# Optimization experiments

Measured on AMD Instinct MI355X. Metric: run time of the kernel, lower is better.

Reference implementation:

```python
import jax, jax.numpy as jnp
import numpy as np
import math

B_GRAPHS = 256
L_NODES = 64
N_NODES = B_GRAPHS * L_NODES
N_EDGES = N_NODES * 4
HEADS = 8
D_INNER = 512
N_DAGS = 1
DIAMETER = 64


def setup_inputs() -> dict:
    key = jax.random.key(0)
    ks = jax.random.split(key, 8)
    x = jax.random.normal(ks[0], (N_NODES, D_INNER), jnp.float32)
    B = jax.random.normal(ks[1], (N_NODES, D_INNER), jnp.float32)
    C = jax.random.normal(ks[2], (N_NODES, D_INNER), jnp.float32)
    dt = jax.random.normal(ks[3], (N_NODES, N_DAGS * HEADS * 2), jnp.float32)
    dt_edge = jax.random.normal(ks[4], (N_EDGES, N_DAGS * HEADS), jnp.float32)
    # DAG edges: within each graph, src_local < dst_local (gap 1..7) -> strictly upper triangular
    u = jax.random.randint(ks[5], (N_EDGES,), 0, L_NODES - 1)
    gap = jax.random.randint(ks[6], (N_EDGES,), 1, 8)
    v = jnp.minimum(u + gap, L_NODES - 1)
    graph = jnp.arange(N_EDGES) // (N_EDGES // B_GRAPHS)
    edge_index = jnp.stack([graph * L_NODES + u, graph * L_NODES + v]).astype(jnp.int32)
    data_batch = (jnp.arange(N_NODES) // L_NODES).astype(jnp.int32)
    dag_masks = jnp.ones((N_DAGS, N_EDGES), jnp.float32)
    # dt_bias init as in module __init__ (inverse softplus of dt in [1e-3, 1e-1])
    rng = np.random.default_rng(0)
    dtv = np.exp(rng.uniform(size=(HEADS,)) * (math.log(0.1) - math.log(0.001)) + math.log(0.001))
    dtv = np.clip(dtv, 1e-4, None)
    dt_bias = jnp.asarray(dtv + np.log(-np.expm1(-dtv)), jnp.float32)
    D = jnp.ones((HEADS,), jnp.float32)
    return dict(x=x, B=B, C=C, dt=dt, dt_edge=dt_edge, dt_bias=dt_bias, D=D,
                dag_masks=dag_masks, edge_index=edge_index, data_batch=data_batch,
                diameter=DIAMETER)


def _repeated_squaring_inverse(A, diam):
    # (I - A)^{-1} = prod_k (I + A^{2^k}) for nilpotent A; O(log diam) matmuls
    j = 2 ** int(math.ceil(math.log2(diam)))
    I = jnp.eye(A.shape[-1], dtype=A.dtype)
    last = A
    M = I + A
    for _ in range(2, int(math.log2(j)) + 1):
        last = last @ last
        M = M @ (I + last)
    return M


def reference(x, B, C, dt, dt_edge, dt_bias, D, dag_masks, edge_index, data_batch, diameter):
    N, din = x.shape
    g, E = dag_masks.shape
    n = dt_bias.shape[0]
    b = int(data_batch[-1]) + 1
    l = N // b  # equal-size graphs -> dense batching is a reshape, mask all-True
    h = din // n
    src, dst = edge_index[0], edge_index[1]

    # dt_node: (N, g*n*c) -> (c, g, n, N); softplus(dt + bias)
    c = dt.shape[1] // (g * n)
    dtn = dt.reshape(N, g, n, c).transpose(3, 1, 2, 0)
    dtn = jax.nn.softplus(dtn + dt_bias[None, None, :, None])
    dte = dt_edge.reshape(E, g, n).transpose(1, 2, 0)  # (g,n,E)
    dte = jax.nn.softplus(dte + dt_bias[None, :, None])

    dt_s, dt_t = dtn[0], dtn[1]
    dt_sum = (dt_s[:, :, src] + dt_t[:, :, dst] + dte) / np.sqrt(3.0)  # (g,n,E)
    dt_exp = jnp.exp(-dt_sum)
    msk = dag_masks[:, None, :]
    dt_sum = dt_sum * msk
    dt_exp = dt_exp * msk

    # dense adjacency with per-edge attrs; note 'b l1 l2 (g n) -> b g n l2 l1' transpose
    b_e = src // l
    sl = src % l
    dl = dst % l
    attr = dt_exp.transpose(2, 0, 1).reshape(E, g * n)
    adj = jnp.zeros((b, l, l, g * n), x.dtype).at[b_e, sl, dl].add(attr)
    A = adj.reshape(b, l, l, g, n).transpose(0, 3, 4, 2, 1)  # (b,g,n,l,l)

    # normalize_mat: sqrt outer product of in-degree counts, clamped at 1
    ec = jnp.zeros((g, N), x.dtype).at[:, dst].add(dag_masks)
    ec_dense = ec.T.reshape(b, l, g)
    outer = jnp.sqrt(jnp.einsum('blg,btg->bglt', ec_dense, ec_dense))
    outer = jnp.where(outer < 1.0, 1.0, outer)
    A = A / outer[:, :, None]

    dnorm = jnp.zeros((g, n, N), x.dtype).at[:, :, dst].add(dt_sum)
    dnorm = dnorm.transpose(2, 0, 1).reshape(b, l, g, n).transpose(0, 2, 3, 1)  # (b,g,n,l)

    A2 = A.reshape(b, g * n, l, l).astype(jnp.float32)
    L = _repeated_squaring_inverse(A2, int(diameter))
    L = L.reshape(b, g, n, l, l) * dnorm[..., None]

    x4 = x.reshape(b, l, n, h).transpose(0, 2, 1, 3)  # (b,n,l,h)
    B3 = B.reshape(b, l, -1)
    C3 = C.reshape(b, l, -1)
    # y = einsum(C,L,B,x) with B/C broadcast over (g,n): fold C.B^T into L
    CB = jnp.einsum('bld,btd->blt', C3, B3)
    M = L * CB[:, None, None]
    y = jnp.einsum('bgnlt,bnth->bgnlh', M, x4)
    y = y + x4[:, None] * D[None, None, :, None, None]
    y = y.transpose(0, 3, 1, 2, 4).reshape(N, g, n * h)  # b g n l h -> (N, g, n*h)
    y = y.sum(axis=1) / np.sqrt(g)
    return y
```

## Files before the change

kernel.cpp:

```cpp
#include <hip/hip_runtime.h>
#include <math.h>

#define NGRAPH 256
#define LNODE  64
#define HEADS  8
#define DIN    512
#define EPG    256
#define NEDGE  65536

__device__ __forceinline__ float softplusf(float v) {
    return (v > 20.f) ? v : log1pf(expf(v));
}

__global__ __launch_bounds__(256) void cb_kernel(const float* __restrict__ Bm,
                                                 const float* __restrict__ Cm,
                                                 float* __restrict__ CBt,
                                                 int dper) {
    int b = blockIdx.x;
    int slice = blockIdx.y;
    __shared__ float Rs[64 * 68];
    __shared__ float Ls[64 * 68];
    int tid = threadIdx.x;
    int ti = tid >> 4, tj = tid & 15;
    float acc[4][4] = {};
    const float* Bg = Bm + (size_t)b * 64 * DIN;
    const float* Cg = Cm + (size_t)b * 64 * DIN;
    int d_lo = slice * dper;
    for (int d0 = d_lo; d0 < d_lo + dper; d0 += 64) {
        __syncthreads();
        #pragma unroll
        for (int k = 0; k < 4; ++k) {
            int f = k * 256 + tid;
            int row = f >> 4;
            int c4 = (f & 15) << 2;
            float4 bv = *(const float4*)(Bg + row * DIN + d0 + c4);
            float4 cv = *(const float4*)(Cg + row * DIN + d0 + c4);
            *(float4*)(Rs + row * 68 + c4) = bv;
            *(float4*)(Ls + row * 68 + c4) = cv;
        }
        __syncthreads();
        for (int d = 0; d < 64; d += 4) {
            float4 rr[4], cc[4];
            #pragma unroll
            for (int r = 0; r < 4; ++r) rr[r] = *(const float4*)(Rs + (4 * ti + r) * 68 + d);
            #pragma unroll
            for (int c = 0; c < 4; ++c) cc[c] = *(const float4*)(Ls + (4 * tj + c) * 68 + d);
            #pragma unroll
            for (int r = 0; r < 4; ++r)
                #pragma unroll
                for (int c = 0; c < 4; ++c)
                    acc[r][c] += rr[r].x * cc[c].x + rr[r].y * cc[c].y +
                                 rr[r].z * cc[c].z + rr[r].w * cc[c].w;
        }
    }
    float* outp = CBt + ((size_t)slice * NGRAPH + b) * 4096;
    #pragma unroll
    for (int r = 0; r < 4; ++r) {
        float4 v = make_float4(acc[r][0], acc[r][1], acc[r][2], acc[r][3]);
        *(float4*)(outp + (4 * ti + r) * 64 + 4 * tj) = v;
    }
}

__global__ __launch_bounds__(256, 4) void main_kernel(const float* __restrict__ x,
                                                      const float* __restrict__ dt,
                                                      const float* __restrict__ dt_edge,
                                                      const float* __restrict__ dt_bias,
                                                      const float* __restrict__ Dp,
                                                      const float* __restrict__ dag_masks,
                                                      const int* __restrict__ edge_index,
                                                      const float* __restrict__ CBt,
                                                      float* __restrict__ out,
                                                      int nslice) {
    int b = blockIdx.x;
    int head = blockIdx.y;
    __shared__ float Ab[64 * 8];
    __shared__ float Mt[64 * 68];
    __shared__ float Xs[64 * 64];
    __shared__ float dnsh[64];
    __shared__ float ecsh[64];
    __shared__ float dts[64];
    __shared__ float dtt[64];
    int tid = threadIdx.x;

    int t4 = tid >> 2;
    int ib = (tid & 3) << 4;
    float4 cbsum[4];
    #pragma unroll
    for (int g = 0; g < 4; ++g) cbsum[g] = make_float4(0.f, 0.f, 0.f, 0.f);
    for (int s = 0; s < nslice; ++s) {
        const float* p = CBt + ((size_t)s * NGRAPH + b) * 4096 + t4 * 64 + ib;
        float4 v0 = *(const float4*)(p + 0);
        float4 v1 = *(const float4*)(p + 4);
        float4 v2 = *(const float4*)(p + 8);
        float4 v3 = *(const float4*)(p + 12);
        cbsum[0].x += v0.x; cbsum[0].y += v0.y; cbsum[0].z += v0.z; cbsum[0].w += v0.w;
        cbsum[1].x += v1.x; cbsum[1].y += v1.y; cbsum[1].z += v1.z; cbsum[1].w += v1.w;
        cbsum[2].x += v2.x; cbsum[2].y += v2.y; cbsum[2].z += v2.z; cbsum[2].w += v2.w;
        cbsum[3].x += v3.x; cbsum[3].y += v3.y; cbsum[3].z += v3.z; cbsum[3].w += v3.w;
    }

    const float* xg0 = x + ((size_t)b * 64) * DIN + head * 64;
    #pragma unroll
    for (int k = 0; k < 4; ++k) {
        int s = k * 256 + tid;
        int row = s >> 4;
        int c4 = (s & 15) << 2;
        float4 v = *(const float4*)(xg0 + (size_t)row * DIN + c4);
        *(float4*)(Xs + row * 64 + c4) = v;
    }

    for (int k = tid; k < 512; k += 256) Ab[k] = 0.f;
    float bias = dt_bias[head];
    if (tid < 64) {
        dnsh[tid] = 0.f;
        ecsh[tid] = 0.f;
        int node = b * 64 + tid;
        dts[tid] = softplusf(dt[node * 16 + head * 2 + 0] + bias);
        dtt[tid] = softplusf(dt[node * 16 + head * 2 + 1] + bias);
    }
    __syncthreads();

    {
        int e = b * EPG + tid;
        int src = edge_index[e];
        int dst = edge_index[NEDGE + e];
        int sl = src & 63;
        int dl = dst & 63;
        float m = dag_masks[e];
        float de = softplusf(dt_edge[e * HEADS + head] + bias);
        float dsum = (dts[sl] + dtt[dl] + de) * 0.57735026918962576451f;
        float dexp = expf(-dsum);
        atomicAdd(&Ab[dl * 8 + (dl - sl)], dexp * m);
        atomicAdd(&dnsh[dl], dsum * m);
        atomicAdd(&ecsh[dl], m);
    }
    __syncthreads();

    for (int k = tid; k < 512; k += 256) {
        int i = k >> 3, d = k & 7;
        int src = i - d;
        if (d >= 1 && src >= 0) {
            float denom = sqrtf(ecsh[i] * ecsh[src]);
            if (denom < 1.f) denom = 1.f;
            Ab[k] = Ab[k] / denom;
        }
    }
    __syncthreads();

    if (tid < 64) {
        int j = tid;
        float mwin[7] = {0.f, 0.f, 0.f, 0.f, 0.f, 0.f, 0.f};
        for (int i = 0; i < 64; ++i) {
            float mi = (j == i) ? 1.f : 0.f;
            #pragma unroll
            for (int s = 0; s < 7; ++s) {
                if (i - 1 - s >= 0) mi += Ab[i * 8 + s + 1] * mwin[s];
            }
            Mt[j * 65 + i] = mi;
            #pragma unroll
            for (int s = 6; s > 0; --s) mwin[s] = mwin[s - 1];
            mwin[0] = mi;
        }
    }
    __syncthreads();

    {
        float w[16];
        #pragma unroll
        for (int g = 0; g < 4; ++g) {
            float4 dn4 = *(const float4*)(dnsh + ib + 4 * g);
            w[4 * g + 0] = Mt[t4 * 65 + ib + 4 * g + 0] * cbsum[g].x * dn4.x;
            w[4 * g + 1] = Mt[t4 * 65 + ib + 4 * g + 1] * cbsum[g].y * dn4.y;
            w[4 * g + 2] = Mt[t4 * 65 + ib + 4 * g + 2] * cbsum[g].z * dn4.z;
            w[4 * g + 3] = Mt[t4 * 65 + ib + 4 * g + 3] * cbsum[g].w * dn4.w;
        }
        __syncthreads();
        #pragma unroll
        for (int g = 0; g < 4; ++g) {
            *(float4*)(Mt + t4 * 68 + ib + 4 * g) =
                make_float4(w[4 * g + 0], w[4 * g + 1], w[4 * g + 2], w[4 * g + 3]);
        }
    }
    __syncthreads();

    int ti = tid >> 4, tj = tid & 15;
    float acc[4][4] = {};
    #pragma unroll 4
    for (int t = 0; t < 64; ++t) {
        float4 w4 = *(const float4*)(Mt + t * 68 + 4 * ti);
        float4 xv = *(const float4*)(Xs + t * 64 + 4 * tj);
        acc[0][0] += w4.x * xv.x; acc[0][1] += w4.x * xv.y; acc[0][2] += w4.x * xv.z; acc[0][3] += w4.x * xv.w;
        acc[1][0] += w4.y * xv.x; acc[1][1] += w4.y * xv.y; acc[1][2] += w4.y * xv.z; acc[1][3] += w4.y * xv.w;
        acc[2][0] += w4.z * xv.x; acc[2][1] += w4.z * xv.y; acc[2][2] += w4.z * xv.z; acc[2][3] += w4.z * xv.w;
        acc[3][0] += w4.w * xv.x; acc[3][1] += w4.w * xv.y; acc[3][2] += w4.w * xv.z; acc[3][3] += w4.w * xv.w;
    }
    float Dh = Dp[head];
    #pragma unroll
    for (int r = 0; r < 4; ++r) {
        int i = 4 * ti + r;
        float4 xres = *(const float4*)(Xs + i * 64 + 4 * tj);
        float4 v;
        v.x = acc[r][0] + xres.x * Dh;
        v.y = acc[r][1] + xres.y * Dh;
        v.z = acc[r][2] + xres.z * Dh;
        v.w = acc[r][3] + xres.w * Dh;
        *(float4*)(out + ((size_t)(b * 64 + i)) * DIN + head * 64 + 4 * tj) = v;
    }
}

extern "C" void kernel_launch(void* const* d_in, const int* in_sizes, int n_in,
                              void* d_out, int out_size, void* d_ws, size_t ws_size,
                              hipStream_t stream) {
    const float* x        = (const float*)d_in[0];
    const float* Bm       = (const float*)d_in[1];
    const float* Cm       = (const float*)d_in[2];
    const float* dt       = (const float*)d_in[3];
    const float* dt_edge  = (const float*)d_in[4];
    const float* dt_bias  = (const float*)d_in[5];
    const float* Dp       = (const float*)d_in[6];
    const float* dag_mask = (const float*)d_in[7];
    const int*   edge_idx = (const int*)d_in[8];
    float* out = (float*)d_out;
    float* CBt = (float*)d_ws;

    int nslice = (ws_size >= (size_t)4 * NGRAPH * 4096 * 4) ? 4 : 1;
    int dper = DIN / nslice;

    cb_kernel<<<dim3(NGRAPH, nslice), 256, 0, stream>>>(Bm, Cm, CBt, dper);
    main_kernel<<<dim3(NGRAPH, HEADS), 256, 0, stream>>>(x, dt, dt_edge, dt_bias, Dp,
                                                         dag_mask, edge_idx, CBt, out, nslice);
}
```

Before: 194.8 us.

## Split main kernel into prep and bf16-weight GEMM kernels

Splits the per-(graph,head) work into a prep kernel and a GEMM kernel. The prep kernel builds the transfer matrix with one wavefront per head, folding in CB, dnorm and the D skip term, and stores it as bf16 in the workspace. The GEMM kernel then only loads the bf16 weights and x, so the serial 64-step recurrence on a single wave no longer stalls the matmul blocks. The cost is an extra launch, a global round trip of the weight matrix, and bf16 rounding error in the weights. A fused fallback is kept for when the workspace is too small.

```diff
diff --git a/kernel.cpp b/kernel.cpp
--- a/kernel.cpp
+++ b/kernel.cpp
@@ -11,20 +11,29 @@
 __device__ __forceinline__ float softplusf(float v) {
     return (v > 20.f) ? v : log1pf(expf(v));
 }
+__device__ __forceinline__ unsigned short f2bf(float f) {
+    union { float f; unsigned u; } c; c.f = f;
+    unsigned r = c.u + 0x7fffu + ((c.u >> 16) & 1u);
+    return (unsigned short)(r >> 16);
+}
+__device__ __forceinline__ float bf2f(unsigned short h) {
+    union { float f; unsigned u; } c; c.u = ((unsigned)h) << 16;
+    return c.f;
+}
 
 __global__ __launch_bounds__(256) void cb_kernel(const float* __restrict__ Bm,
                                                  const float* __restrict__ Cm,
-                                                 float* __restrict__ CBt,
-                                                 int dper) {
+                                                 float* __restrict__ CBp,
+                                                 int dper, int tposed) {
     int b = blockIdx.x;
     int slice = blockIdx.y;
-    __shared__ float Rs[64 * 68];
-    __shared__ float Ls[64 * 68];
+    __shared__ float Cs[64 * 68];
+    __shared__ float Bs[64 * 68];
     int tid = threadIdx.x;
     int ti = tid >> 4, tj = tid & 15;
     float acc[4][4] = {};
+    const float* Cg = Cm + (size_t)b * 64 * DIN;
     const float* Bg = Bm + (size_t)b * 64 * DIN;
-    const float* Cg = Cm + (size_t)b * 64 * DIN;
     int d_lo = slice * dper;
     for (int d0 = d_lo; d0 < d_lo + dper; d0 += 64) {
         __syncthreads();
@@ -33,44 +42,211 @@
             int f = k * 256 + tid;
             int row = f >> 4;
             int c4 = (f & 15) << 2;
-            float4 bv = *(const float4*)(Bg + row * DIN + d0 + c4);
-            float4 cv = *(const float4*)(Cg + row * DIN + d0 + c4);
-            *(float4*)(Rs + row * 68 + c4) = bv;
-            *(float4*)(Ls + row * 68 + c4) = cv;
+            *(float4*)(Cs + row * 68 + c4) = *(const float4*)(Cg + row * DIN + d0 + c4);
+            *(float4*)(Bs + row * 68 + c4) = *(const float4*)(Bg + row * DIN + d0 + c4);
         }
         __syncthreads();
         for (int d = 0; d < 64; d += 4) {
-            float4 rr[4], cc[4];
-            #pragma unroll
-            for (int r = 0; r < 4; ++r) rr[r] = *(const float4*)(Rs + (4 * ti + r) * 68 + d);
-            #pragma unroll
-            for (int c = 0; c < 4; ++c) cc[c] = *(const float4*)(Ls + (4 * tj + c) * 68 + d);
+            float4 cr[4], br[4];
+            #pragma unroll
+            for (int r = 0; r < 4; ++r) cr[r] = *(const float4*)(Cs + (4 * ti + r) * 68 + d);
+            #pragma unroll
+            for (int c = 0; c < 4; ++c) br[c] = *(const float4*)(Bs + (4 * tj + c) * 68 + d);
             #pragma unroll
             for (int r = 0; r < 4; ++r)
                 #pragma unroll
                 for (int c = 0; c < 4; ++c)
-                    acc[r][c] += rr[r].x * cc[c].x + rr[r].y * cc[c].y +
-                                 rr[r].z * cc[c].z + rr[r].w * cc[c].w;
-        }
-    }
-    float* outp = CBt + ((size_t)slice * NGRAPH + b) * 4096;
+                    acc[r][c] += cr[r].x * br[c].x + cr[r].y * br[c].y +
+                                 cr[r].z * br[c].z + cr[r].w * br[c].w;
+        }
+    }
+    float* outp = CBp + ((size_t)slice * NGRAPH + b) * 4096;
+    if (!tposed) {
+        #pragma unroll
+        for (int r = 0; r < 4; ++r)
+            *(float4*)(outp + (4 * ti + r) * 64 + 4 * tj) =
+                make_float4(acc[r][0], acc[r][1], acc[r][2], acc[r][3]);
+    } else {
+        #pragma unroll
+        for (int r = 0; r < 4; ++r)
+            #pragma unroll
+            for (int c = 0; c < 4; ++c)
+                outp[(4 * tj + c) * 64 + (4 * ti + r)] = acc[r][c];
+    }
+}
+
+__global__ __launch_bounds__(256) void prep_kernel(const float* __restrict__ dt,
+                                                   const float* __restrict__ dt_edge,
+                                                   const float* __restrict__ dt_bias,
+                                                   const float* __restrict__ Dp,
+                                                   const float* __restrict__ dag_masks,
+                                                   const int* __restrict__ edge_index,
+                                                   const float* __restrict__ CBp,
+                                                   unsigned short* __restrict__ Wtg,
+                                                   int nslice) {
+    int b = blockIdx.x;
+    int hq = blockIdx.y;
+    int tid = threadIdx.x;
+    int w = tid >> 6;
+    int lane = tid & 63;
+    int head = hq * 4 + w;
+
+    __shared__ float CBsh[4096];
+    __shared__ unsigned short Wt[4][4096];
+    __shared__ float Ab[4][512];
+    __shared__ float dnsh[4][64];
+    __shared__ float dts[4][64];
+    __shared__ float dtt[4][64];
+    __shared__ float ecsh[4][64];
+
+    for (int s4 = tid; s4 < 1024; s4 += 256) {
+        float4 v = make_float4(0.f, 0.f, 0.f, 0.f);
+        for (int s = 0; s < nslice; ++s) {
+            float4 p = *(const float4*)(CBp + ((size_t)s * NGRAPH + b) * 4096 + s4 * 4);
+            v.x += p.x; v.y += p.y; v.z += p.z; v.w += p.w;
+        }
+        *(float4*)(CBsh + s4 * 4) = v;
+    }
+    #pragma unroll
+    for (int k = 0; k < 8; ++k) Ab[w][k * 64 + lane] = 0.f;
+    dnsh[w][lane] = 0.f;
+    ecsh[w][lane] = 0.f;
+    float bias = dt_bias[head];
+    {
+        int node = b * 64 + lane;
+        dts[w][lane] = softplusf(dt[node * 16 + head * 2 + 0] + bias);
+        dtt[w][lane] = softplusf(dt[node * 16 + head * 2 + 1] + bias);
+    }
+    __syncthreads();
+
+    #pragma unroll
+    for (int k = 0; k < 4; ++k) {
+        int e = b * EPG + k * 64 + lane;
+        int sl = edge_index[e] & 63;
+        int dl = edge_index[NEDGE + e] & 63;
+        float m = dag_masks[e];
+        float de = softplusf(dt_edge[e * HEADS + head] + bias);
+        float dsum = (dts[w][sl] + dtt[w][dl] + de) * 0.57735026918962576451f;
+        float dexp = expf(-dsum);
+        atomicAdd(&Ab[w][dl * 8 + (dl - sl)], dexp * m);
+        atomicAdd(&dnsh[w][dl], dsum * m);
+        atomicAdd(&ecsh[w][dl], m);
+    }
+
+    {
+        float eci = ecsh[w][lane];
+        #pragma unroll
+        for (int d = 1; d < 8; ++d) {
+            int s_ = lane - d;
+            if (s_ >= 0) {
+                float den = sqrtf(eci * ecsh[w][s_]);
+                if (den < 1.f) den = 1.f;
+                Ab[w][lane * 8 + d] = Ab[w][lane * 8 + d] / den;
+            }
+        }
+    }
+
+    {
+        int j = lane;
+        float Dh = Dp[head];
+        float mwin[7] = {0.f, 0.f, 0.f, 0.f, 0.f, 0.f, 0.f};
+        for (int i8 = 0; i8 < 8; ++i8) {
+            unsigned pk[4];
+            #pragma unroll
+            for (int u = 0; u < 8; ++u) {
+                int i = i8 * 8 + u;
+                float mi = (j == i) ? 1.f : 0.f;
+                #pragma unroll
+                for (int s = 0; s < 7; ++s) mi += Ab[w][i * 8 + s + 1] * mwin[s];
+                float wv = mi * CBsh[i * 64 + j] * dnsh[w][i];
+                if (j == i) wv += Dh;
+                #pragma unroll
+                for (int s = 6; s > 0; --s) mwin[s] = mwin[s - 1];
+                mwin[0] = mi;
+                unsigned short hb = f2bf(wv);
+                if (u & 1) pk[u >> 1] |= ((unsigned)hb) << 16;
+                else       pk[u >> 1] = (unsigned)hb;
+            }
+            int cblk = i8 ^ (j & 7);
+            *(uint4*)(&Wt[w][j * 64 + cblk * 8]) = make_uint4(pk[0], pk[1], pk[2], pk[3]);
+        }
+    }
+    __syncthreads();
+
+    {
+        size_t ghbase = ((size_t)b * HEADS + head) * 4096;
+        int r_off = lane >> 3;
+        int ibk = lane & 7;
+        #pragma unroll
+        for (int r0 = 0; r0 < 64; r0 += 8) {
+            int r = r0 + r_off;
+            int cblk = ibk ^ (r & 7);
+            uint4 v = *(const uint4*)(&Wt[w][r * 64 + cblk * 8]);
+            *(uint4*)(Wtg + ghbase + (size_t)r * 64 + ibk * 8) = v;
+        }
+    }
+}
+
+__global__ __launch_bounds__(256) void gemm_kernel(const float* __restrict__ x,
+                                                   const unsigned short* __restrict__ Wtg,
+                                                   float* __restrict__ out) {
+    int b = blockIdx.x;
+    int head = blockIdx.y;
+    __shared__ unsigned short Wt[64 * 72];
+    __shared__ float Xs[64 * 64];
+    int tid = threadIdx.x;
+
+    const uint4* wg = (const uint4*)(Wtg + ((size_t)b * HEADS + head) * 4096);
+    #pragma unroll
+    for (int q = 0; q < 2; ++q) {
+        int s = q * 256 + tid;
+        int row = s >> 3;
+        int c8 = (s & 7) * 8;
+        *(uint4*)(&Wt[row * 72 + c8]) = wg[s];
+    }
+    const float* xg0 = x + (size_t)b * 64 * DIN + head * 64;
+    #pragma unroll
+    for (int k = 0; k < 4; ++k) {
+        int s = k * 256 + tid;
+        int row = s >> 4;
+        int c4 = (s & 15) << 2;
+        *(float4*)(Xs + row * 64 + c4) = *(const float4*)(xg0 + (size_t)row * DIN + c4);
+    }
+    __syncthreads();
+
+    int ti = tid >> 4, tj = tid & 15;
+    float acc[4][4] = {};
+    #pragma unroll 4
+    for (int t = 0; t < 64; ++t) {
+        uint2 wp = *(const uint2*)(&Wt[t * 72 + 4 * ti]);
+        float w0 = bf2f((unsigned short)(wp.x & 0xffffu));
+        float w1 = bf2f((unsigned short)(wp.x >> 16));
+        float w2 = bf2f((unsigned short)(wp.y & 0xffffu));
+        float w3 = bf2f((unsigned short)(wp.y >> 16));
+        float4 xv = *(const float4*)(Xs + t * 64 + 4 * tj);
+        acc[0][0] += w0 * xv.x; acc[0][1] += w0 * xv.y; acc[0][2] += w0 * xv.z; acc[0][3] += w0 * xv.w;
+        acc[1][0] += w1 * xv.x; acc[1][1] += w1 * xv.y; acc[1][2] += w1 * xv.z; acc[1][3] += w1 * xv.w;
+        acc[2][0] += w2 * xv.x; acc[2][1] += w2 * xv.y; acc[2][2] += w2 * xv.z; acc[2][3] += w2 * xv.w;
+        acc[3][0] += w3 * xv.x; acc[3][1] += w3 * xv.y; acc[3][2] += w3 * xv.z; acc[3][3] += w3 * xv.w;
+    }
     #pragma unroll
     for (int r = 0; r < 4; ++r) {
-        float4 v = make_float4(acc[r][0], acc[r][1], acc[r][2], acc[r][3]);
-        *(float4*)(outp + (4 * ti + r) * 64 + 4 * tj) = v;
-    }
-}
-
-__global__ __launch_bounds__(256, 4) void main_kernel(const float* __restrict__ x,
-                                                      const float* __restrict__ dt,
-                                                      const float* __restrict__ dt_edge,
-                                                      const float* __restrict__ dt_bias,
-                                                      const float* __restrict__ Dp,
-                                                      const float* __restrict__ dag_masks,
-                                                      const int* __restrict__ edge_index,
-                                                      const float* __restrict__ CBt,
-                                                      float* __restrict__ out,
-                                                      int nslice) {
+        int i = 4 * ti + r;
+        *(float4*)(out + ((size_t)(b * 64 + i)) * DIN + head * 64 + 4 * tj) =
+            make_float4(acc[r][0], acc[r][1], acc[r][2], acc[r][3]);
+    }
+}
+
+__global__ __launch_bounds__(256, 4) void fused_kernel(const float* __restrict__ x,
+                                                       const float* __restrict__ dt,
+                                                       const float* __restrict__ dt_edge,
+                                                       const float* __restrict__ dt_bias,
+                                                       const float* __restrict__ Dp,
+                                                       const float* __restrict__ dag_masks,
+                                                       const int* __restrict__ edge_index,
+                                                       const float* __restrict__ CBt,
+                                                       float* __restrict__ out,
+                                                       int nslice) {
     int b = blockIdx.x;
     int head = blockIdx.y;
     __shared__ float Ab[64 * 8];
@@ -89,26 +265,20 @@
     for (int g = 0; g < 4; ++g) cbsum[g] = make_float4(0.f, 0.f, 0.f, 0.f);
     for (int s = 0; s < nslice; ++s) {
         const float* p = CBt + ((size_t)s * NGRAPH + b) * 4096 + t4 * 64 + ib;
-        float4 v0 = *(const float4*)(p + 0);
-        float4 v1 = *(const float4*)(p + 4);
-        float4 v2 = *(const float4*)(p + 8);
-        float4 v3 = *(const float4*)(p + 12);
-        cbsum[0].x += v0.x; cbsum[0].y += v0.y; cbsum[0].z += v0.z; cbsum[0].w += v0.w;
-        cbsum[1].x += v1.x; cbsum[1].y += v1.y; cbsum[1].z += v1.z; cbsum[1].w += v1.w;
-        cbsum[2].x += v2.x; cbsum[2].y += v2.y; cbsum[2].z += v2.z; cbsum[2].w += v2.w;
-        cbsum[3].x += v3.x; cbsum[3].y += v3.y; cbsum[3].z += v3.z; cbsum[3].w += v3.w;
-    }
-
+        #pragma unroll
+        for (int g = 0; g < 4; ++g) {
+            float4 v = *(const float4*)(p + 4 * g);
+            cbsum[g].x += v.x; cbsum[g].y += v.y; cbsum[g].z += v.z; cbsum[g].w += v.w;
+        }
+    }
     const float* xg0 = x + ((size_t)b * 64) * DIN + head * 64;
     #pragma unroll
     for (int k = 0; k < 4; ++k) {
         int s = k * 256 + tid;
         int row = s >> 4;
         int c4 = (s & 15) << 2;
-        float4 v = *(const float4*)(xg0 + (size_t)row * DIN + c4);
-        *(float4*)(Xs + row * 64 + c4) = v;
-    }
-
+        *(float4*)(Xs + row * 64 + c4) = *(const float4*)(xg0 + (size_t)row * DIN + c4);
+    }
     for (int k = tid; k < 512; k += 256) Ab[k] = 0.f;
     float bias = dt_bias[head];
     if (tid < 64) {
@@ -119,13 +289,10 @@
         dtt[tid] = softplusf(dt[node * 16 + head * 2 + 1] + bias);
     }
     __syncthreads();
-
     {
         int e = b * EPG + tid;
-        int src = edge_index[e];
-        int dst = edge_index[NEDGE + e];
-        int sl = src & 63;
-        int dl = dst & 63;
+        int sl = edge_index[e] & 63;
+        int dl = edge_index[NEDGE + e] & 63;
         float m = dag_masks[e];
         float de = softplusf(dt_edge[e * HEADS + head] + bias);
         float dsum = (dts[sl] + dtt[dl] + de) * 0.57735026918962576451f;
@@ -135,27 +302,23 @@
         atomicAdd(&ecsh[dl], m);
     }
     __syncthreads();
-
     for (int k = tid; k < 512; k += 256) {
         int i = k >> 3, d = k & 7;
         int src = i - d;
         if (d >= 1 && src >= 0) {
-            float denom = sqrtf(ecsh[i] * ecsh[src]);
-            if (denom < 1.f) denom = 1.f;
-            Ab[k] = Ab[k] / denom;
-        }
-    }
-    __syncthreads();
-
+            float den = sqrtf(ecsh[i] * ecsh[src]);
+            if (den < 1.f) den = 1.f;
+            Ab[k] = Ab[k] / den;
+        }
+    }
+    __syncthreads();
     if (tid < 64) {
         int j = tid;
         float mwin[7] = {0.f, 0.f, 0.f, 0.f, 0.f, 0.f, 0.f};
         for (int i = 0; i < 64; ++i) {
             float mi = (j == i) ? 1.f : 0.f;
             #pragma unroll
-            for (int s = 0; s < 7; ++s) {
-                if (i - 1 - s >= 0) mi += Ab[i * 8 + s + 1] * mwin[s];
-            }
+            for (int s = 0; s < 7; ++s) mi += Ab[i * 8 + s + 1] * mwin[s];
             Mt[j * 65 + i] = mi;
             #pragma unroll
             for (int s = 6; s > 0; --s) mwin[s] = mwin[s - 1];
@@ -163,26 +326,23 @@
         }
     }
     __syncthreads();
-
-    {
-        float w[16];
+    {
+        float wv[16];
         #pragma unroll
         for (int g = 0; g < 4; ++g) {
             float4 dn4 = *(const float4*)(dnsh + ib + 4 * g);
-            w[4 * g + 0] = Mt[t4 * 65 + ib + 4 * g + 0] * cbsum[g].x * dn4.x;
-            w[4 * g + 1] = Mt[t4 * 65 + ib + 4 * g + 1] * cbsum[g].y * dn4.y;
-            w[4 * g + 2] = Mt[t4 * 65 + ib + 4 * g + 2] * cbsum[g].z * dn4.z;
-            w[4 * g + 3] = Mt[t4 * 65 + ib + 4 * g + 3] * cbsum[g].w * dn4.w;
+            wv[4 * g + 0] = Mt[t4 * 65 + ib + 4 * g + 0] * cbsum[g].x * dn4.x;
+            wv[4 * g + 1] = Mt[t4 * 65 + ib + 4 * g + 1] * cbsum[g].y * dn4.y;
+            wv[4 * g + 2] = Mt[t4 * 65 + ib + 4 * g + 2] * cbsum[g].z * dn4.z;
+            wv[4 * g + 3] = Mt[t4 * 65 + ib + 4 * g + 3] * cbsum[g].w * dn4.w;
         }
         __syncthreads();
         #pragma unroll
-        for (int g = 0; g < 4; ++g) {
+        for (int g = 0; g < 4; ++g)
             *(float4*)(Mt + t4 * 68 + ib + 4 * g) =
-                make_float4(w[4 * g + 0], w[4 * g + 1], w[4 * g + 2], w[4 * g + 3]);
-        }
-    }
-    __syncthreads();
-
+                make_float4(wv[4 * g + 0], wv[4 * g + 1], wv[4 * g + 2], wv[4 * g + 3]);
+    }
+    __syncthreads();
     int ti = tid >> 4, tj = tid & 15;
     float acc[4][4] = {};
     #pragma unroll 4
@@ -221,12 +381,29 @@
     const float* dag_mask = (const float*)d_in[7];
     const int*   edge_idx = (const int*)d_in[8];
     float* out = (float*)d_out;
-    float* CBt = (float*)d_ws;
-
-    int nslice = (ws_size >= (size_t)4 * NGRAPH * 4096 * 4) ? 4 : 1;
+
+    const size_t CBSLICE = (size_t)NGRAPH * 4096 * 4;
+    const size_t WBYTES  = (size_t)NGRAPH * HEADS * 4096 * 2;
+
+    int nslice;
+    bool fused;
+    if (ws_size >= WBYTES + 4 * CBSLICE)      { fused = false; nslice = 4; }
+    else if (ws_size >= WBYTES + 2 * CBSLICE) { fused = false; nslice = 2; }
+    else if (ws_size >= WBYTES + 1 * CBSLICE) { fused = false; nslice = 1; }
+    else { fused = true; nslice = (ws_size >= 4 * CBSLICE) ? 4 : 1; }
+
+    float* CBp = (float*)d_ws;
     int dper = DIN / nslice;
 
-    cb_kernel<<<dim3(NGRAPH, nslice), 256, 0, stream>>>(Bm, Cm, CBt, dper);
-    main_kernel<<<dim3(NGRAPH, HEADS), 256, 0, stream>>>(x, dt, dt_edge, dt_bias, Dp,
-                                                         dag_mask, edge_idx, CBt, out, nslice);
-}
+    if (!fused) {
+        unsigned short* Wtg = (unsigned short*)((char*)d_ws + nslice * CBSLICE);
+        cb_kernel<<<dim3(NGRAPH, nslice), 256, 0, stream>>>(Bm, Cm, CBp, dper, 0);
+        prep_kernel<<<dim3(NGRAPH, 2), 256, 0, stream>>>(dt, dt_edge, dt_bias, Dp,
+                                                         dag_mask, edge_idx, CBp, Wtg, nslice);
+        gemm_kernel<<<dim3(NGRAPH, HEADS), 256, 0, stream>>>(x, Wtg, out);
+    } else {
+        cb_kernel<<<dim3(NGRAPH, nslice), 256, 0, stream>>>(Bm, Cm, CBp, dper, 1);
+        fused_kernel<<<dim3(NGRAPH, HEADS), 256, 0, stream>>>(x, dt, dt_edge, dt_bias, Dp,
+                                                              dag_mask, edge_idx, CBp, out, nslice);
+    }
+}
```

Result: no change. 193.3 us (-0.8%).
